# Optimization experiments

Measured on AMD Instinct MI355X. Metric: run time of the kernel, lower is better.

## Reference

```python
import jax, jax.numpy as jnp
import numpy as np

B, S, D, H = 2, 2048, 1024, 16
HD = D // H
EPS = 1e-5


def _layernorm(x, g, b):
    mu = jnp.mean(x, axis=-1, keepdims=True)
    var = jnp.mean(jnp.square(x - mu), axis=-1, keepdims=True)
    return (x - mu) * jax.lax.rsqrt(var + EPS) * g + b


def setup_inputs() -> dict:
    key = jax.random.key(0)
    ks = jax.random.split(key, 12)
    s = 1.0 / np.sqrt(D)
    return {
        "x": jax.random.normal(ks[0], (B, S, D), jnp.float32),
        "Wq": jax.random.uniform(ks[1], (D, D), jnp.float32, -s, s),
        "bq": jax.random.uniform(ks[2], (D,), jnp.float32, -s, s),
        "Wk": jax.random.uniform(ks[3], (D, D), jnp.float32, -s, s),
        "bk": jax.random.uniform(ks[4], (D,), jnp.float32, -s, s),
        "Wv": jax.random.uniform(ks[5], (D, D), jnp.float32, -s, s),
        "bv": jax.random.uniform(ks[6], (D,), jnp.float32, -s, s),
        "ln_g": jnp.ones((D,), jnp.float32),
        "ln_b": jnp.zeros((D,), jnp.float32),
        "W1": jax.random.uniform(ks[7], (D, D), jnp.float32, -s, s),
        "b1": jax.random.uniform(ks[8], (D,), jnp.float32, -s, s),
        "W2": jax.random.uniform(ks[9], (D, D), jnp.float32, -s, s),
        "b2": jax.random.uniform(ks[10], (D,), jnp.float32, -s, s),
    }


def reference(x, Wq, bq, Wk, bk, Wv, bv, ln_g, ln_b, W1, b1, W2, b2):
    # QKV projections (torch Linear: x @ W.T + b), split into heads -> [B,H,S,HD]
    q = (x @ Wq.T + bq).reshape(B, S, H, HD).transpose(0, 2, 1, 3)
    k = (x @ Wk.T + bk).reshape(B, S, H, HD).transpose(0, 2, 1, 3)
    v = (x @ Wv.T + bv).reshape(B, S, H, HD).transpose(0, 2, 1, 3)
    # Full score matrix [B,H,S,S] (faithful to unfused original)
    scores = jnp.einsum("bhqd,bhkd->bhqk", q, k) / np.sqrt(HD).astype(np.float32)
    attn = jax.nn.softmax(scores, axis=-1)  # dropout = identity (eval mode)
    ctx = jnp.einsum("bhqk,bhkd->bhqd", attn, v)
    ctx = ctx.transpose(0, 2, 1, 3).reshape(B, S, D)
    ctx = _layernorm(ctx + x, ln_g, ln_b)
    ffn = jax.nn.relu(ctx @ W1.T + b1) @ W2.T + b2
    return _layernorm(ffn + ctx, ln_g, ln_b)
```

## Files before the change

kernel.cpp:

```cpp
#include <hip/hip_runtime.h>
#include <stdint.h>

#define D_MODEL 1024
#define NHEAD   16
#define HDIM    64
#define BATCH   2
#define SEQ     2048
#define NTOK    (BATCH*SEQ)

typedef unsigned short u16;
typedef unsigned int   u32;
typedef __attribute__((ext_vector_type(8)))  short bf16x8;
typedef __attribute__((ext_vector_type(8)))  u16   u16x8;
typedef __attribute__((ext_vector_type(4)))  u16   u16x4;
typedef __attribute__((ext_vector_type(4)))  u32   u32x4;
typedef __attribute__((ext_vector_type(4)))  float f32x4;
typedef __attribute__((ext_vector_type(16))) float f32x16;

#if __has_builtin(__builtin_amdgcn_exp2f)
#define EXP2F __builtin_amdgcn_exp2f
#else
#define EXP2F exp2f
#endif

__device__ __forceinline__ u16 f2bf(float f) {
  uint32_t u = __float_as_uint(f);
  u += 0x7fffu + ((u >> 16) & 1u);
  return (u16)(u >> 16);
}

__device__ __forceinline__ void gl_lds16(const u16* g, u16* l) {
  __builtin_amdgcn_global_load_lds(
      (const __attribute__((address_space(1))) void*)g,
      (__attribute__((address_space(3))) void*)l, 16, 0, 0);
}

__device__ __forceinline__ u32 cvtpk(float lo, float hi) {
  u32 r;
  asm("v_cvt_pk_bf16_f32 %0, %1, %2" : "=v"(r) : "v"(lo), "v"(hi));
  return r;
}
__device__ __forceinline__ void pl32swap(u32& a, u32& b) {
  asm("v_permlane32_swap_b32 %0, %1" : "+v"(a), "+v"(b));
}

__device__ __forceinline__ f32x16 mfma32(bf16x8 a, bf16x8 b, f32x16 c) {
  return __builtin_amdgcn_mfma_f32_32x32x16_bf16(a, b, c, 0, 0, 0);
}

__global__ __launch_bounds__(256) void cvt_kernel(const float* __restrict__ in,
                                                  u16* __restrict__ out, int n) {
  int i = (blockIdx.x * 256 + threadIdx.x) * 8;
  if (i >= n) return;
  float4 a = *(const float4*)(in + i);
  float4 b = *(const float4*)(in + i + 4);
  u16x8 o;
  o[0] = f2bf(a.x); o[1] = f2bf(a.y); o[2] = f2bf(a.z); o[3] = f2bf(a.w);
  o[4] = f2bf(b.x); o[5] = f2bf(b.y); o[6] = f2bf(b.z); o[7] = f2bf(b.w);
  *(u16x8*)(out + i) = o;
}

template <int EPI>
__global__ __launch_bounds__(256) void gemm_bt(const u16* __restrict__ A,
                                               const u16* __restrict__ B,
                                               const float* __restrict__ bias,
                                               void* __restrict__ C,
                                               int M, int N, int K) {
  __shared__ u16 a_lds[128 * 32];
  __shared__ u16 b_lds[128 * 32];
  const int t = threadIdx.x;
  const int l = t & 63;
  const int w = t >> 6;
  const int wr = w >> 1, wc = w & 1;
  const int bm = blockIdx.y * 128, bn = blockIdx.x * 128;
  const int fl = l & 15, fh = l >> 4;

  f32x4 acc[4][4] = {};

  const int row0 = t >> 2;
  const int row1 = (t + 256) >> 2;
  const int col0 = (t & 3) * 8;

  for (int k0 = 0; k0 < K; k0 += 32) {
    __syncthreads();
    gl_lds16(A + (size_t)(bm + row0) * K + k0 + col0, &a_lds[t * 8]);
    gl_lds16(A + (size_t)(bm + row1) * K + k0 + col0, &a_lds[(t + 256) * 8]);
    gl_lds16(B + (size_t)(bn + row0) * K + k0 + col0, &b_lds[t * 8]);
    gl_lds16(B + (size_t)(bn + row1) * K + k0 + col0, &b_lds[(t + 256) * 8]);
    __syncthreads();

    bf16x8 af[4], bf[4];
#pragma unroll
    for (int mi = 0; mi < 4; ++mi)
      af[mi] = *(const bf16x8*)&a_lds[(wr * 64 + mi * 16 + fl) * 32 + fh * 8];
#pragma unroll
    for (int ni = 0; ni < 4; ++ni)
      bf[ni] = *(const bf16x8*)&b_lds[(wc * 64 + ni * 16 + fl) * 32 + fh * 8];
#pragma unroll
    for (int mi = 0; mi < 4; ++mi)
#pragma unroll
      for (int ni = 0; ni < 4; ++ni)
        acc[mi][ni] = __builtin_amdgcn_mfma_f32_16x16x32_bf16(
            af[mi], bf[ni], acc[mi][ni], 0, 0, 0);
  }

#pragma unroll
  for (int mi = 0; mi < 4; ++mi) {
#pragma unroll
    for (int ni = 0; ni < 4; ++ni) {
      const int col = bn + wc * 64 + ni * 16 + fl;
      const float bv = bias ? bias[col] : 0.f;
#pragma unroll
      for (int r = 0; r < 4; ++r) {
        const int row = bm + wr * 64 + mi * 16 + fh * 4 + r;
        float v = acc[mi][ni][r] + bv;
        if (EPI == 0) {
          ((float*)C)[(size_t)row * N + col] = v;
        } else if (EPI == 1) {
          ((u16*)C)[(size_t)row * N + col] = f2bf(v);
        } else {
          ((u16*)C)[(size_t)row * N + col] = f2bf(fmaxf(v, 0.f));
        }
      }
    }
  }
}

__global__ __launch_bounds__(256) void transpose_v(const u16* __restrict__ qkv,
                                                   u16* __restrict__ vT) {
  __shared__ u16 tile[64][72];
  const int t = threadIdx.x;
  const int s0 = blockIdx.x * 64;
  const int bh = blockIdx.y, b = bh >> 4, h = bh & 15;
#pragma unroll
  for (int cc = 0; cc < 2; ++cc) {
    int idx = t + cc * 256, row = idx >> 3, c = idx & 7;
    *(bf16x8*)&tile[row][c * 8] = *(const bf16x8*)(
        qkv + (size_t)(b * SEQ + s0 + row) * 3072 + 2048 + h * 64 + c * 8);
  }
  __syncthreads();
#pragma unroll
  for (int cc = 0; cc < 2; ++cc) {
    int idx = t + cc * 256, drow = idx >> 3, c = idx & 7;
    u16x8 o;
#pragma unroll
    for (int j = 0; j < 8; ++j) o[j] = tile[c * 8 + j][drow];
    *(u16x8*)(vT + (size_t)(bh * 64 + drow) * SEQ + s0 + c * 8) = o;
  }
}

__global__ __launch_bounds__(256, 2) void attn_kernel(const u16* __restrict__ qkv,
                                                      const u16* __restrict__ vT,
                                                      float* __restrict__ ctx) {
  __shared__ u16 kbuf[2][64 * 64];
  __shared__ u16 vbuf[2][64 * 64];
  __shared__ float o_stage[4][32][68];

  const int t = threadIdx.x, l = t & 63, w = t >> 6;
  const int r0 = l & 31, hi = l >> 5, hib = hi * 16;

  const int id = blockIdx.x;
  const int swz = (id & 7) * 64 + (id >> 3);
  const int qblk = swz & 15;
  const int bh = swz >> 4;
  const int b = bh >> 4, h = bh & 15;
  const int q0 = qblk * 128;
  const size_t rowbase = (size_t)b * SEQ;

  bf16x8 qf[4];
#pragma unroll
  for (int kd = 0; kd < 4; ++kd)
    qf[kd] = *(const bf16x8*)(qkv +
        (rowbase + q0 + w * 32 + r0) * 3072 + h * 64 + kd * 16 + hi * 8);

  f32x16 acc[2] = {};
  float m_run = -1e30f, l_run = 0.f;
  const float C = 0.18033688011f;

#define STAGE(bb, kt)                                                          \
  {                                                                            \
    _Pragma("unroll")                                                          \
    for (int cc = 0; cc < 2; ++cc) {                                           \
      int i = t + cc * 256;                                                    \
      int rr = i >> 3, cb = (i & 7) * 16;                                      \
      int sc_ = cb ^ ((rr & 7) << 4);                                          \
      gl_lds16(qkv + (rowbase + (kt) + rr) * 3072 + 1024 + h * 64 + (sc_ >> 1),\
               &kbuf[bb][i * 8]);                                              \
      gl_lds16(vT + ((size_t)bh * 64 + rr) * SEQ + (kt) + (sc_ >> 1),          \
               &vbuf[bb][i * 8]);                                              \
    }                                                                          \
  }

  STAGE(0, 0);
  __syncthreads();

  for (int ti = 0; ti < SEQ / 64; ++ti) {
    const int cur = ti & 1;
    if (ti + 1 < SEQ / 64) STAGE(cur ^ 1, (ti + 1) * 64);

    const u16* kb = kbuf[cur];
    const u16* vb = vbuf[cur];

    f32x16 p0 = {}, p1 = {};
#pragma unroll
    for (int kd = 0; kd < 4; ++kd) {
      const int cb = kd * 32 + hib;
      const uint8_t* pk = (const uint8_t*)kb;
      bf16x8 klo = *(const bf16x8*)(pk + r0 * 128 + (cb ^ ((r0 & 7) << 4)));
      bf16x8 khi = *(const bf16x8*)(pk + (r0 + 32) * 128 + (cb ^ ((r0 & 7) << 4)));
      p0 = mfma32(klo, qf[kd], p0);
      p1 = mfma32(khi, qf[kd], p1);
    }

    float mx0 = fmaxf(p0[0], p0[1]), mx1 = fmaxf(p0[2], p0[3]);
    float mx2 = fmaxf(p1[0], p1[1]), mx3 = fmaxf(p1[2], p1[3]);
#pragma unroll
    for (int i = 4; i < 16; i += 4) {
      mx0 = fmaxf(mx0, fmaxf(p0[i], p0[i + 1]));
      mx1 = fmaxf(mx1, fmaxf(p0[i + 2], p0[i + 3]));
      mx2 = fmaxf(mx2, fmaxf(p1[i], p1[i + 1]));
      mx3 = fmaxf(mx3, fmaxf(p1[i + 2], p1[i + 3]));
    }
    float mloc = fmaxf(fmaxf(mx0, mx1), fmaxf(mx2, mx3));
    mloc = fmaxf(mloc, __shfl_xor(mloc, 32, 64));

    if (!__all(mloc - m_run <= 44.0f)) {
      const float mnew = fmaxf(m_run, mloc);
      const float sc = EXP2F((m_run - mnew) * C);
      m_run = mnew;
      l_run *= sc;
#pragma unroll
      for (int dblk = 0; dblk < 2; ++dblk)
#pragma unroll
        for (int i = 0; i < 16; ++i) acc[dblk][i] *= sc;
    }
    const float mC = m_run * C;
    float ps = 0.f;
#pragma unroll
    for (int i = 0; i < 16; ++i) {
      p0[i] = EXP2F(fmaf(p0[i], C, -mC));
      ps += p0[i];
    }
#pragma unroll
    for (int i = 0; i < 16; ++i) {
      p1[i] = EXP2F(fmaf(p1[i], C, -mC));
      ps += p1[i];
    }
    ps += __shfl_xor(ps, 32, 64);
    l_run += ps;

    bf16x8 pb[4];
    {
      u32 c0, c1, c2, c3;
      u32x4 f;
      c0 = cvtpk(p0[0], p0[1]);  c1 = cvtpk(p0[2], p0[3]);
      c2 = cvtpk(p0[4], p0[5]);  c3 = cvtpk(p0[6], p0[7]);
      pl32swap(c0, c2); pl32swap(c1, c3);
      f[0] = c0; f[1] = c1; f[2] = c2; f[3] = c3; pb[0] = *(bf16x8*)&f;
      c0 = cvtpk(p0[8], p0[9]);  c1 = cvtpk(p0[10], p0[11]);
      c2 = cvtpk(p0[12], p0[13]); c3 = cvtpk(p0[14], p0[15]);
      pl32swap(c0, c2); pl32swap(c1, c3);
      f[0] = c0; f[1] = c1; f[2] = c2; f[3] = c3; pb[1] = *(bf16x8*)&f;
      c0 = cvtpk(p1[0], p1[1]);  c1 = cvtpk(p1[2], p1[3]);
      c2 = cvtpk(p1[4], p1[5]);  c3 = cvtpk(p1[6], p1[7]);
      pl32swap(c0, c2); pl32swap(c1, c3);
      f[0] = c0; f[1] = c1; f[2] = c2; f[3] = c3; pb[2] = *(bf16x8*)&f;
      c0 = cvtpk(p1[8], p1[9]);  c1 = cvtpk(p1[10], p1[11]);
      c2 = cvtpk(p1[12], p1[13]); c3 = cvtpk(p1[14], p1[15]);
      pl32swap(c0, c2); pl32swap(c1, c3);
      f[0] = c0; f[1] = c1; f[2] = c2; f[3] = c3; pb[3] = *(bf16x8*)&f;
    }

#pragma unroll
    for (int dblk = 0; dblk < 2; ++dblk) {
#pragma unroll
      for (int ks = 0; ks < 4; ++ks) {
        const int rr = dblk * 32 + r0;
        const int cb = ks * 32 + hib;
        bf16x8 vf = *(const bf16x8*)((const uint8_t*)vb + rr * 128 +
                                     (cb ^ ((rr & 7) << 4)));
        acc[dblk] = mfma32(vf, pb[ks], acc[dblk]);
      }
    }
    __syncthreads();
  }

  const float invl = 1.f / l_run;
#pragma unroll
  for (int dblk = 0; dblk < 2; ++dblk)
#pragma unroll
    for (int i = 0; i < 16; ++i) {
      const int d = dblk * 32 + (i & 3) + 8 * (i >> 2) + 4 * hi;
      o_stage[w][r0][d] = acc[dblk][i] * invl;
    }
#pragma unroll
  for (int it = 0; it < 8; ++it) {
    const int r = it * 4 + (l >> 4);
    const int c = (l & 15) * 4;
    const float4 v = *(const float4*)&o_stage[w][r][c];
    *(float4*)&ctx[(rowbase + q0 + w * 32 + r) * D_MODEL + h * 64 + c] = v;
  }
#undef STAGE
}

__global__ __launch_bounds__(256) void ln_kernel(const float* __restrict__ a,
                                                 const float* __restrict__ res,
                                                 const float* __restrict__ g,
                                                 const float* __restrict__ bta,
                                                 float* __restrict__ outf,
                                                 u16* __restrict__ outb) {
  __shared__ float sbuf[4];
  const int t = threadIdx.x;
  const size_t row = blockIdx.x;
  const float4 va = *(const float4*)(a + row * 1024 + t * 4);
  const float4 vr = *(const float4*)(res + row * 1024 + t * 4);
  float v[4] = {va.x + vr.x, va.y + vr.y, va.z + vr.z, va.w + vr.w};
  float s = v[0] + v[1] + v[2] + v[3];
#pragma unroll
  for (int m = 32; m; m >>= 1) s += __shfl_xor(s, m, 64);
  if ((t & 63) == 0) sbuf[t >> 6] = s;
  __syncthreads();
  const float mean = (sbuf[0] + sbuf[1] + sbuf[2] + sbuf[3]) * (1.f / 1024.f);
  float q = 0.f;
#pragma unroll
  for (int i = 0; i < 4; ++i) { v[i] -= mean; q += v[i] * v[i]; }
#pragma unroll
  for (int m = 32; m; m >>= 1) q += __shfl_xor(q, m, 64);
  __syncthreads();
  if ((t & 63) == 0) sbuf[t >> 6] = q;
  __syncthreads();
  const float var = (sbuf[0] + sbuf[1] + sbuf[2] + sbuf[3]) * (1.f / 1024.f);
  const float rs = rsqrtf(var + 1e-5f);
  const float4 vg = *(const float4*)(g + t * 4);
  const float4 vb = *(const float4*)(bta + t * 4);
  float o[4];
  o[0] = v[0] * rs * vg.x + vb.x;
  o[1] = v[1] * rs * vg.y + vb.y;
  o[2] = v[2] * rs * vg.z + vb.z;
  o[3] = v[3] * rs * vg.w + vb.w;
  float4 of = {o[0], o[1], o[2], o[3]};
  *(float4*)(outf + row * 1024 + t * 4) = of;
  if (outb) {
    u16x4 ob;
#pragma unroll
    for (int i = 0; i < 4; ++i) ob[i] = f2bf(o[i]);
    *(u16x4*)(outb + row * 1024 + t * 4) = ob;
  }
}

extern "C" void kernel_launch(void* const* d_in, const int* in_sizes, int n_in,
                              void* d_out, int out_size, void* d_ws, size_t ws_size,
                              hipStream_t stream) {
  const float* x    = (const float*)d_in[0];
  const float* Wq   = (const float*)d_in[1];
  const float* bq   = (const float*)d_in[2];
  const float* Wk   = (const float*)d_in[3];
  const float* bk   = (const float*)d_in[4];
  const float* Wv   = (const float*)d_in[5];
  const float* bv   = (const float*)d_in[6];
  const float* ln_g = (const float*)d_in[7];
  const float* ln_b = (const float*)d_in[8];
  const float* W1   = (const float*)d_in[9];
  const float* b1   = (const float*)d_in[10];
  const float* W2   = (const float*)d_in[11];
  const float* b2   = (const float*)d_in[12];
  float* out = (float*)d_out;

  uint8_t* ws = (uint8_t*)d_ws;
  const size_t MB = 1 << 20;
  u16*   x_bf  = (u16*)  (ws + 0 * MB);
  u16*   wqkv  = (u16*)  (ws + 8 * MB);
  u16*   w1b   = (u16*)  (ws + 14 * MB);
  u16*   w2b   = (u16*)  (ws + 16 * MB);
  float* bqkv  = (float*)(ws + 18 * MB);
  u16*   qkv   = (u16*)  (ws + 19 * MB);
  u16*   vT    = (u16*)  (ws + 43 * MB);
  float* ctx   = (float*)(ws + 51 * MB);
  float* y     = (float*)(ws + 67 * MB);
  u16*   y_bf  = (u16*)  (ws + 83 * MB);
  u16*   h1    = (u16*)  (ws + 91 * MB);
  float* ffn   = (float*)(ws + 99 * MB);

  hipMemcpyAsync(bqkv,        bq, 1024 * sizeof(float), hipMemcpyDeviceToDevice, stream);
  hipMemcpyAsync(bqkv + 1024, bk, 1024 * sizeof(float), hipMemcpyDeviceToDevice, stream);
  hipMemcpyAsync(bqkv + 2048, bv, 1024 * sizeof(float), hipMemcpyDeviceToDevice, stream);

  cvt_kernel<<<2048, 256, 0, stream>>>(x, x_bf, NTOK * D_MODEL);
  cvt_kernel<<<512, 256, 0, stream>>>(Wq, wqkv, 1 << 20);
  cvt_kernel<<<512, 256, 0, stream>>>(Wk, wqkv + (1 << 20), 1 << 20);
  cvt_kernel<<<512, 256, 0, stream>>>(Wv, wqkv + (2 << 20), 1 << 20);
  cvt_kernel<<<512, 256, 0, stream>>>(W1, w1b, 1 << 20);
  cvt_kernel<<<512, 256, 0, stream>>>(W2, w2b, 1 << 20);

  gemm_bt<1><<<dim3(24, 32), 256, 0, stream>>>(x_bf, wqkv, bqkv, qkv,
                                               NTOK, 3072, 1024);
  transpose_v<<<dim3(32, 32), 256, 0, stream>>>(qkv, vT);
  attn_kernel<<<512, 256, 0, stream>>>(qkv, vT, ctx);
  ln_kernel<<<4096, 256, 0, stream>>>(ctx, x, ln_g, ln_b, y, y_bf);
  gemm_bt<2><<<dim3(8, 32), 256, 0, stream>>>(y_bf, w1b, b1, h1,
                                              NTOK, 1024, 1024);
  gemm_bt<0><<<dim3(8, 32), 256, 0, stream>>>(h1, w2b, b2, ffn,
                                              NTOK, 1024, 1024);
  ln_kernel<<<4096, 256, 0, stream>>>(ffn, y, ln_g, ln_b, out, nullptr);
}
```

Baseline: 281.6 us.

## Split attention KV range across waves, fuse conversions, swizzle GEMM block order

Attention now uses 64-query blocks, with two wave pairs each handling half of the KV sequence. Partial results are merged through LDS at the end, which doubles the grid and raises occupancy to 4 blocks per CU. The aim is more parallelism and better latency hiding, but it drops the double-buffered prefetch and adds extra syncs. All weight and input conversions plus the bias copies are fused into one kernel to cut launch overhead. GEMMs get a 1D grid with an XCD-aware swizzle, and s_setprio is wrapped around the MFMA sections.

```diff
diff --git a/kernel.cpp b/kernel.cpp
--- a/kernel.cpp
+++ b/kernel.cpp
@@ -48,16 +48,35 @@
   return __builtin_amdgcn_mfma_f32_32x32x16_bf16(a, b, c, 0, 0, 0);
 }
 
-__global__ __launch_bounds__(256) void cvt_kernel(const float* __restrict__ in,
-                                                  u16* __restrict__ out, int n) {
-  int i = (blockIdx.x * 256 + threadIdx.x) * 8;
-  if (i >= n) return;
-  float4 a = *(const float4*)(in + i);
-  float4 b = *(const float4*)(in + i + 4);
+__global__ __launch_bounds__(256) void cvt_all(
+    const float* __restrict__ x,  const float* __restrict__ Wq,
+    const float* __restrict__ Wk, const float* __restrict__ Wv,
+    const float* __restrict__ W1, const float* __restrict__ W2,
+    const float* __restrict__ bq, const float* __restrict__ bk,
+    const float* __restrict__ bv,
+    u16* __restrict__ x_bf, u16* __restrict__ wqkv,
+    u16* __restrict__ w1b,  u16* __restrict__ w2b,
+    float* __restrict__ bqkv) {
+  const int bid = blockIdx.x, t = threadIdx.x;
+  if (bid == 4608) {
+    for (int i = t; i < 3072; i += 256)
+      bqkv[i] = i < 1024 ? bq[i] : (i < 2048 ? bk[i - 1024] : bv[i - 2048]);
+    return;
+  }
+  const float* src; u16* dst; int off;
+  if (bid < 2048)      { src = x;  dst = x_bf;            off = bid; }
+  else if (bid < 2560) { src = Wq; dst = wqkv;            off = bid - 2048; }
+  else if (bid < 3072) { src = Wk; dst = wqkv + (1 << 20); off = bid - 2560; }
+  else if (bid < 3584) { src = Wv; dst = wqkv + (2 << 20); off = bid - 3072; }
+  else if (bid < 4096) { src = W1; dst = w1b;             off = bid - 3584; }
+  else                 { src = W2; dst = w2b;             off = bid - 4096; }
+  const int i = (off * 256 + t) * 8;
+  float4 a = *(const float4*)(src + i);
+  float4 b = *(const float4*)(src + i + 4);
   u16x8 o;
   o[0] = f2bf(a.x); o[1] = f2bf(a.y); o[2] = f2bf(a.z); o[3] = f2bf(a.w);
   o[4] = f2bf(b.x); o[5] = f2bf(b.y); o[6] = f2bf(b.z); o[7] = f2bf(b.w);
-  *(u16x8*)(out + i) = o;
+  *(u16x8*)(dst + i) = o;
 }
 
 template <int EPI>
@@ -72,7 +91,10 @@
   const int l = t & 63;
   const int w = t >> 6;
   const int wr = w >> 1, wc = w & 1;
-  const int bm = blockIdx.y * 128, bn = blockIdx.x * 128;
+  const int gxn = N >> 7;
+  const int cpx = gridDim.x >> 3;
+  const int swz = (blockIdx.x & 7) * cpx + (blockIdx.x >> 3);
+  const int bm = (swz / gxn) * 128, bn = (swz % gxn) * 128;
   const int fl = l & 15, fh = l >> 4;
 
   f32x4 acc[4][4] = {};
@@ -149,59 +171,59 @@
   }
 }
 
-__global__ __launch_bounds__(256, 2) void attn_kernel(const u16* __restrict__ qkv,
+__global__ __launch_bounds__(256, 4) void attn_kernel(const u16* __restrict__ qkv,
                                                       const u16* __restrict__ vT,
                                                       float* __restrict__ ctx) {
-  __shared__ u16 kbuf[2][64 * 64];
-  __shared__ u16 vbuf[2][64 * 64];
-  __shared__ float o_stage[4][32][68];
+  __shared__ u16 smem[4][64 * 64];
+  __shared__ float mlbuf[2][2][32][2];
 
   const int t = threadIdx.x, l = t & 63, w = t >> 6;
   const int r0 = l & 31, hi = l >> 5, hib = hi * 16;
+  const int qg = w >> 1, hfv = w & 1;
 
   const int id = blockIdx.x;
-  const int swz = (id & 7) * 64 + (id >> 3);
-  const int qblk = swz & 15;
-  const int bh = swz >> 4;
+  const int swz = (id & 7) * 128 + (id >> 3);
+  const int qblk = swz & 31;
+  const int bh = swz >> 5;
   const int b = bh >> 4, h = bh & 15;
-  const int q0 = qblk * 128;
+  const int q0 = qblk * 64;
   const size_t rowbase = (size_t)b * SEQ;
 
   bf16x8 qf[4];
 #pragma unroll
   for (int kd = 0; kd < 4; ++kd)
     qf[kd] = *(const bf16x8*)(qkv +
-        (rowbase + q0 + w * 32 + r0) * 3072 + h * 64 + kd * 16 + hi * 8);
+        (rowbase + q0 + qg * 32 + r0) * 3072 + h * 64 + kd * 16 + hi * 8);
 
   f32x16 acc[2] = {};
   float m_run = -1e30f, l_run = 0.f;
   const float C = 0.18033688011f;
 
-#define STAGE(bb, kt)                                                          \
-  {                                                                            \
-    _Pragma("unroll")                                                          \
-    for (int cc = 0; cc < 2; ++cc) {                                           \
-      int i = t + cc * 256;                                                    \
-      int rr = i >> 3, cb = (i & 7) * 16;                                      \
-      int sc_ = cb ^ ((rr & 7) << 4);                                          \
-      gl_lds16(qkv + (rowbase + (kt) + rr) * 3072 + 1024 + h * 64 + (sc_ >> 1),\
-               &kbuf[bb][i * 8]);                                              \
-      gl_lds16(vT + ((size_t)bh * 64 + rr) * SEQ + (kt) + (sc_ >> 1),          \
-               &vbuf[bb][i * 8]);                                              \
-    }                                                                          \
-  }
-
-  STAGE(0, 0);
-  __syncthreads();
-
-  for (int ti = 0; ti < SEQ / 64; ++ti) {
-    const int cur = ti & 1;
-    if (ti + 1 < SEQ / 64) STAGE(cur ^ 1, (ti + 1) * 64);
-
-    const u16* kb = kbuf[cur];
-    const u16* vb = vbuf[cur];
+  const u16* kb = smem[hfv * 2 + 0];
+  const u16* vb = smem[hfv * 2 + 1];
+
+  for (int s = 0; s < 16; ++s) {
+    __syncthreads();
+#pragma unroll
+    for (int cc = 0; cc < 8; ++cc) {
+      const int i = t + cc * 256;
+      const int arr = i >> 9;
+      const int j = i & 511;
+      const int rr = j >> 3, cb = (j & 7) * 16;
+      const int sc_ = cb ^ ((rr & 7) << 4);
+      const int hv = arr >> 1;
+      u16* dst = &smem[arr][j * 8];
+      if ((arr & 1) == 0)
+        gl_lds16(qkv + (rowbase + hv * 1024 + s * 64 + rr) * 3072 + 1024 +
+                     h * 64 + (sc_ >> 1), dst);
+      else
+        gl_lds16(vT + ((size_t)bh * 64 + rr) * SEQ + hv * 1024 + s * 64 +
+                     (sc_ >> 1), dst);
+    }
+    __syncthreads();
 
     f32x16 p0 = {}, p1 = {};
+    __builtin_amdgcn_s_setprio(1);
 #pragma unroll
     for (int kd = 0; kd < 4; ++kd) {
       const int cb = kd * 32 + hib;
@@ -211,6 +233,7 @@
       p0 = mfma32(klo, qf[kd], p0);
       p1 = mfma32(khi, qf[kd], p1);
     }
+    __builtin_amdgcn_s_setprio(0);
 
     float mx0 = fmaxf(p0[0], p0[1]), mx1 = fmaxf(p0[2], p0[3]);
     float mx2 = fmaxf(p1[0], p1[1]), mx3 = fmaxf(p1[2], p1[3]);
@@ -253,24 +276,25 @@
     {
       u32 c0, c1, c2, c3;
       u32x4 f;
-      c0 = cvtpk(p0[0], p0[1]);  c1 = cvtpk(p0[2], p0[3]);
-      c2 = cvtpk(p0[4], p0[5]);  c3 = cvtpk(p0[6], p0[7]);
+      c0 = cvtpk(p0[0], p0[1]);   c1 = cvtpk(p0[2], p0[3]);
+      c2 = cvtpk(p0[4], p0[5]);   c3 = cvtpk(p0[6], p0[7]);
       pl32swap(c0, c2); pl32swap(c1, c3);
       f[0] = c0; f[1] = c1; f[2] = c2; f[3] = c3; pb[0] = *(bf16x8*)&f;
-      c0 = cvtpk(p0[8], p0[9]);  c1 = cvtpk(p0[10], p0[11]);
+      c0 = cvtpk(p0[8], p0[9]);   c1 = cvtpk(p0[10], p0[11]);
       c2 = cvtpk(p0[12], p0[13]); c3 = cvtpk(p0[14], p0[15]);
       pl32swap(c0, c2); pl32swap(c1, c3);
       f[0] = c0; f[1] = c1; f[2] = c2; f[3] = c3; pb[1] = *(bf16x8*)&f;
-      c0 = cvtpk(p1[0], p1[1]);  c1 = cvtpk(p1[2], p1[3]);
-      c2 = cvtpk(p1[4], p1[5]);  c3 = cvtpk(p1[6], p1[7]);
+      c0 = cvtpk(p1[0], p1[1]);   c1 = cvtpk(p1[2], p1[3]);
+      c2 = cvtpk(p1[4], p1[5]);   c3 = cvtpk(p1[6], p1[7]);
       pl32swap(c0, c2); pl32swap(c1, c3);
       f[0] = c0; f[1] = c1; f[2] = c2; f[3] = c3; pb[2] = *(bf16x8*)&f;
-      c0 = cvtpk(p1[8], p1[9]);  c1 = cvtpk(p1[10], p1[11]);
+      c0 = cvtpk(p1[8], p1[9]);   c1 = cvtpk(p1[10], p1[11]);
       c2 = cvtpk(p1[12], p1[13]); c3 = cvtpk(p1[14], p1[15]);
       pl32swap(c0, c2); pl32swap(c1, c3);
       f[0] = c0; f[1] = c1; f[2] = c2; f[3] = c3; pb[3] = *(bf16x8*)&f;
     }
 
+    __builtin_amdgcn_s_setprio(1);
 #pragma unroll
     for (int dblk = 0; dblk < 2; ++dblk) {
 #pragma unroll
@@ -282,25 +306,51 @@
         acc[dblk] = mfma32(vf, pb[ks], acc[dblk]);
       }
     }
-    __syncthreads();
-  }
-
-  const float invl = 1.f / l_run;
-#pragma unroll
-  for (int dblk = 0; dblk < 2; ++dblk)
-#pragma unroll
-    for (int i = 0; i < 16; ++i) {
-      const int d = dblk * 32 + (i & 3) + 8 * (i >> 2) + 4 * hi;
-      o_stage[w][r0][d] = acc[dblk][i] * invl;
-    }
-#pragma unroll
-  for (int it = 0; it < 8; ++it) {
-    const int r = it * 4 + (l >> 4);
-    const int c = (l & 15) * 4;
-    const float4 v = *(const float4*)&o_stage[w][r][c];
-    *(float4*)&ctx[(rowbase + q0 + w * 32 + r) * D_MODEL + h * 64 + c] = v;
-  }
-#undef STAGE
+    __builtin_amdgcn_s_setprio(0);
+  }
+
+  if (hi == 0) {
+    mlbuf[qg][hfv][r0][0] = m_run;
+    mlbuf[qg][hfv][r0][1] = l_run;
+  }
+  __syncthreads();
+  const float mo  = mlbuf[qg][hfv ^ 1][r0][0];
+  const float lo_ = mlbuf[qg][hfv ^ 1][r0][1];
+  const float mM = fmaxf(m_run, mo);
+  const float sMine = EXP2F((m_run - mM) * C);
+  const float sOth  = EXP2F((mo - mM) * C);
+  const float lM = l_run * sMine + lo_ * sOth;
+
+  float* os = (float*)smem + qg * 32 * 68;
+  if (hfv == 0) {
+#pragma unroll
+    for (int dblk = 0; dblk < 2; ++dblk)
+#pragma unroll
+      for (int i = 0; i < 16; ++i) {
+        const int d = dblk * 32 + (i & 3) + 8 * (i >> 2) + 4 * hi;
+        os[r0 * 68 + d] = acc[dblk][i] * sMine;
+      }
+  }
+  __syncthreads();
+  if (hfv == 1) {
+#pragma unroll
+    for (int dblk = 0; dblk < 2; ++dblk)
+#pragma unroll
+      for (int i = 0; i < 16; ++i) {
+        const int d = dblk * 32 + (i & 3) + 8 * (i >> 2) + 4 * hi;
+        os[r0 * 68 + d] += acc[dblk][i] * sMine;
+      }
+    if (hi == 0) mlbuf[qg][1][r0][1] = 1.f / lM;
+#pragma unroll
+    for (int it = 0; it < 8; ++it) {
+      const int r = it * 4 + (l >> 4);
+      const int c = (l & 15) * 4;
+      const float inv = mlbuf[qg][1][r][1];
+      float4 v = *(const float4*)&os[r * 68 + c];
+      v.x *= inv; v.y *= inv; v.z *= inv; v.w *= inv;
+      *(float4*)&ctx[(rowbase + q0 + qg * 32 + r) * D_MODEL + h * 64 + c] = v;
+    }
+  }
 }
 
 __global__ __launch_bounds__(256) void ln_kernel(const float* __restrict__ a,
@@ -381,25 +431,13 @@
   u16*   h1    = (u16*)  (ws + 91 * MB);
   float* ffn   = (float*)(ws + 99 * MB);
 
-  hipMemcpyAsync(bqkv,        bq, 1024 * sizeof(float), hipMemcpyDeviceToDevice, stream);
-  hipMemcpyAsync(bqkv + 1024, bk, 1024 * sizeof(float), hipMemcpyDeviceToDevice, stream);
-  hipMemcpyAsync(bqkv + 2048, bv, 1024 * sizeof(float), hipMemcpyDeviceToDevice, stream);
-
-  cvt_kernel<<<2048, 256, 0, stream>>>(x, x_bf, NTOK * D_MODEL);
-  cvt_kernel<<<512, 256, 0, stream>>>(Wq, wqkv, 1 << 20);
-  cvt_kernel<<<512, 256, 0, stream>>>(Wk, wqkv + (1 << 20), 1 << 20);
-  cvt_kernel<<<512, 256, 0, stream>>>(Wv, wqkv + (2 << 20), 1 << 20);
-  cvt_kernel<<<512, 256, 0, stream>>>(W1, w1b, 1 << 20);
-  cvt_kernel<<<512, 256, 0, stream>>>(W2, w2b, 1 << 20);
-
-  gemm_bt<1><<<dim3(24, 32), 256, 0, stream>>>(x_bf, wqkv, bqkv, qkv,
-                                               NTOK, 3072, 1024);
+  cvt_all<<<4609, 256, 0, stream>>>(x, Wq, Wk, Wv, W1, W2, bq, bk, bv,
+                                    x_bf, wqkv, w1b, w2b, bqkv);
+  gemm_bt<1><<<768, 256, 0, stream>>>(x_bf, wqkv, bqkv, qkv, NTOK, 3072, 1024);
   transpose_v<<<dim3(32, 32), 256, 0, stream>>>(qkv, vT);
-  attn_kernel<<<512, 256, 0, stream>>>(qkv, vT, ctx);
+  attn_kernel<<<1024, 256, 0, stream>>>(qkv, vT, ctx);
   ln_kernel<<<4096, 256, 0, stream>>>(ctx, x, ln_g, ln_b, y, y_bf);
-  gemm_bt<2><<<dim3(8, 32), 256, 0, stream>>>(y_bf, w1b, b1, h1,
-                                              NTOK, 1024, 1024);
-  gemm_bt<0><<<dim3(8, 32), 256, 0, stream>>>(h1, w2b, b2, ffn,
-                                              NTOK, 1024, 1024);
+  gemm_bt<2><<<256, 256, 0, stream>>>(y_bf, w1b, b1, h1, NTOK, 1024, 1024);
+  gemm_bt<0><<<256, 256, 0, stream>>>(h1, w2b, b2, ffn, NTOK, 1024, 1024);
   ln_kernel<<<4096, 256, 0, stream>>>(ffn, y, ln_g, ln_b, out, nullptr);
 }
```

Result: faster. 273.2 us (-3.0%).
